# Performance work log

Measured on AMD Instinct MI355X. Metric: run time of the kernel, lower is better.

Reference implementation:

```python
import jax, jax.numpy as jnp
import numpy as np

B, S, H, R = 32, 1024, 768, 24
ATT_EPS = 1e10
LN_EPS = 1e-12


def setup_inputs() -> dict:
    key = jax.random.key(0)
    ks = jax.random.split(key, 20)
    sc = 0.02
    inp = {
        "relation": jax.random.randint(ks[0], (B, 1), 0, R),
        "last_hidden_size": jax.random.normal(ks[1], (B, S, H), dtype=jnp.float32),
        "sub_head": jax.random.randint(ks[2], (B, 1), 0, S),
        "sub_tail": jax.random.randint(ks[3], (B, 1), 0, S),
        "attention_mask": jnp.ones((B, S), dtype=jnp.float32),
        # learned parameters
        "rel_emb": jax.random.normal(ks[4], (R, H)) * sc,
        "W_rf": jax.random.normal(ks[5], (H, H)) * sc,
        "b_rf": jnp.zeros((H,), jnp.float32),
        "gamma": jnp.ones((H,), jnp.float32),
        "beta": jnp.zeros((H,), jnp.float32),
        "W_wd": jax.random.normal(ks[6], (H, 2 * H)) * sc,
        "W_bd": jax.random.normal(ks[7], (H, 2 * H)) * sc,
        "Wq": jax.random.normal(ks[8], (H, H)) * sc,
        "bq": jnp.zeros((H,), jnp.float32),
        "Wk": jax.random.normal(ks[9], (H, H)) * sc,
        "bk": jnp.zeros((H,), jnp.float32),
        "Wv": jax.random.normal(ks[10], (H, H)) * sc,
        "bv": jnp.zeros((H,), jnp.float32),
        "W_obj": jax.random.normal(ks[11], (1, H)) * sc,
        "b_obj": jnp.zeros((1,), jnp.float32),
    }
    return inp


def reference(relation, last_hidden_size, sub_head, sub_tail, attention_mask,
              rel_emb, W_rf, b_rf, gamma, beta, W_wd, W_bd,
              Wq, bq, Wk, bk, Wv, bv, W_obj, b_obj):
    # dropout layers are identity in eval mode
    # relation feature: embedding -> linear -> ReLU6   [B,1,H]
    rel_feature = jnp.clip(rel_emb[relation] @ W_rf.T + b_rf, 0.0, 6.0)
    # subject span features via gather                 [B,1,H]
    sh = jnp.take_along_axis(last_hidden_size, sub_head[:, :, None], axis=1)
    st = jnp.take_along_axis(last_hidden_size, sub_tail[:, :, None], axis=1)
    sub_feature = (sh + st) * 0.5
    cond = jnp.concatenate([rel_feature, sub_feature], axis=-1)  # [B,1,2H]

    # conditional layer norm: per-sample affine from condition
    weight = cond @ W_wd.T + gamma  # [B,1,H]
    bias = cond @ W_bd.T + beta     # [B,1,H]
    mean = jnp.mean(last_hidden_size, axis=-1, keepdims=True)
    ctr = last_hidden_size - mean
    var = jnp.mean(ctr * ctr, axis=-1, keepdims=True)
    x = ctr / jnp.sqrt(var + LN_EPS)
    x = x * weight + bias  # [B,S,H]

    # custom attention: ReLU-activated q/k/v, additive mask bias, residual
    q = jax.nn.relu(x @ Wq.T + bq)
    k = jax.nn.relu(x @ Wk.T + bk)
    v = jax.nn.relu(x @ Wv.T + bv)
    e = jnp.einsum('bsh,bth->bst', q, k)  # [B,S,S]
    e = e - ATT_EPS * (1.0 - attention_mask[:, None, :])
    a = jax.nn.softmax(e, axis=-1)
    hidden = jnp.einsum('bst,bth->bsh', a, v) + x  # residual

    pred_obj_head = jnp.squeeze(hidden @ W_obj.T + b_obj, axis=-1)  # [B,S]
    return pred_obj_head, hidden
```

## Files before the change

### kernel.cpp

```cpp
#include <hip/hip_runtime.h>

constexpr int NB  = 32;
constexpr int NS  = 1024;
constexpr int NH  = 768;
constexpr int NH2 = 1536;
constexpr int NQKV = 2304;
constexpr int NBS = NB * NS;

typedef __bf16 bf16x8 __attribute__((ext_vector_type(8)));
typedef float  f32x4  __attribute__((ext_vector_type(4)));
typedef unsigned short u16x8 __attribute__((ext_vector_type(8)));

__device__ __forceinline__ unsigned short f2bf(float f) {
  unsigned int u = __builtin_bit_cast(unsigned int, f);
  u += 0x7FFFu + ((u >> 16) & 1u);
  return (unsigned short)(u >> 16);
}
__device__ __forceinline__ float bf2f(unsigned short h) {
  return __builtin_bit_cast(float, ((unsigned int)h) << 16);
}

#define GLDS16(g, l)                                                         \
  __builtin_amdgcn_global_load_lds(                                          \
      (__attribute__((address_space(1))) void*)(g),                          \
      (__attribute__((address_space(3))) void*)(l), 16, 0, 0)

#define SBAR()    asm volatile("s_barrier" ::: "memory")
#define WAITVM6() asm volatile("s_waitcnt vmcnt(6)" ::: "memory")
#define WAITVM4() asm volatile("s_waitcnt vmcnt(4)" ::: "memory")
#define WAITVM0() asm volatile("s_waitcnt vmcnt(0)" ::: "memory")
#define LGKM0()                                                              \
  do {                                                                       \
    asm volatile("s_waitcnt lgkmcnt(0)" ::: "memory");                       \
    __builtin_amdgcn_sched_barrier(0);                                       \
  } while (0)

__launch_bounds__(256)
__global__ void cond_pre(const int* __restrict__ relation,
                         const float* __restrict__ h,
                         const int* __restrict__ subh,
                         const int* __restrict__ subt,
                         const float* __restrict__ rel_emb,
                         float* __restrict__ reT, float* __restrict__ condT) {
  const int b = blockIdx.x, t = threadIdx.x;
  const int r = relation[b], sh = subh[b], st = subt[b];
  for (int k = t; k < NH; k += 256) {
    reT[(size_t)k * NB + b] = rel_emb[(size_t)r * NH + k];
    condT[(size_t)(NH + k) * NB + b] =
        0.5f * (h[((size_t)b * NS + sh) * NH + k] +
                h[((size_t)b * NS + st) * NH + k]);
  }
}

__launch_bounds__(256)
__global__ void cond_rf(const float* __restrict__ W_rf,
                        const float* __restrict__ b_rf,
                        const float* __restrict__ reT,
                        float* __restrict__ condT) {
  const int t = threadIdx.x;
  const int b = t & 31, jl = t >> 5;
  const int j = blockIdx.x * 8 + jl;
  const float4* w4 = (const float4*)(W_rf + (size_t)j * NH);
  const float* rT = reT + b;
  float a0 = 0.f, a1 = 0.f;
  for (int k4 = 0; k4 < NH / 4; k4++) {
    float4 w = w4[k4];
    const float* c = rT + (size_t)(k4 * 4) * NB;
    a0 += w.x * c[0] + w.y * c[NB];
    a1 += w.z * c[2 * NB] + w.w * c[3 * NB];
  }
  float acc = a0 + a1 + b_rf[j];
  condT[(size_t)j * NB + b] = fminf(fmaxf(acc, 0.0f), 6.0f);
}

__launch_bounds__(256)
__global__ void cond_wb(const float* __restrict__ W_wd,
                        const float* __restrict__ W_bd,
                        const float* __restrict__ gamma,
                        const float* __restrict__ beta,
                        const float* __restrict__ condT,
                        float* __restrict__ wt, float* __restrict__ bs) {
  __shared__ float redW[128], redB[128];
  const int t = threadIdx.x;
  const int b = t & 31, jl = (t >> 5) & 3, ks = t >> 7;
  const int j = blockIdx.x * 4 + jl;
  const float4* ww = (const float4*)(W_wd + (size_t)j * NH2 + ks * NH);
  const float4* wb = (const float4*)(W_bd + (size_t)j * NH2 + ks * NH);
  const float* cT = condT + (size_t)ks * NH * NB + b;
  float aw0 = 0.f, aw1 = 0.f, ab0 = 0.f, ab1 = 0.f;
  for (int k4 = 0; k4 < NH / 4; k4++) {
    float4 w = ww[k4];
    float4 v = wb[k4];
    const float* c = cT + (size_t)(k4 * 4) * NB;
    float c0 = c[0], c1 = c[NB], c2 = c[2 * NB], c3 = c[3 * NB];
    aw0 += w.x * c0 + w.y * c1;
    aw1 += w.z * c2 + w.w * c3;
    ab0 += v.x * c0 + v.y * c1;
    ab1 += v.z * c2 + v.w * c3;
  }
  float aw = aw0 + aw1, ab = ab0 + ab1;
  if (ks == 1) {
    redW[t - 128] = aw;
    redB[t - 128] = ab;
  }
  __syncthreads();
  if (ks == 0) {
    aw += redW[t];
    ab += redB[t];
    wt[(size_t)b * NH + j] = aw + gamma[j];
    bs[(size_t)b * NH + j] = ab + beta[j];
  }
}

__launch_bounds__(64)
__global__ void ln_kernel(const float* __restrict__ h,
                          const float* __restrict__ wt,
                          const float* __restrict__ bs,
                          unsigned short* __restrict__ xbf) {
  const int row = blockIdx.x;
  const int b = row >> 10;
  const int lane = threadIdx.x;
  const float4* hr = (const float4*)(h + (size_t)row * NH);
  float4 v0 = hr[lane], v1 = hr[lane + 64], v2 = hr[lane + 128];
  float sum = 0.f, sq = 0.f;
  {
    sum += v0.x + v0.y + v0.z + v0.w;
    sq  += v0.x * v0.x + v0.y * v0.y + v0.z * v0.z + v0.w * v0.w;
    sum += v1.x + v1.y + v1.z + v1.w;
    sq  += v1.x * v1.x + v1.y * v1.y + v1.z * v1.z + v1.w * v1.w;
    sum += v2.x + v2.y + v2.z + v2.w;
    sq  += v2.x * v2.x + v2.y * v2.y + v2.z * v2.z + v2.w * v2.w;
  }
  for (int off = 32; off > 0; off >>= 1) {
    sum += __shfl_xor(sum, off, 64);
    sq  += __shfl_xor(sq, off, 64);
  }
  const float mean = sum * (1.0f / NH);
  const float var  = sq * (1.0f / NH) - mean * mean;
  const float rstd = rsqrtf(var + 1e-12f);
  const float4* wr = (const float4*)(wt + (size_t)b * NH);
  const float4* br = (const float4*)(bs + (size_t)b * NH);
  ushort4* xr = (ushort4*)(xbf + (size_t)row * NH);
#pragma unroll
  for (int i = 0; i < 3; i++) {
    float4 v = (i == 0) ? v0 : (i == 1) ? v1 : v2;
    float4 w = wr[lane + 64 * i];
    float4 bb = br[lane + 64 * i];
    ushort4 o;
    o.x = f2bf((v.x - mean) * rstd * w.x + bb.x);
    o.y = f2bf((v.y - mean) * rstd * w.y + bb.y);
    o.z = f2bf((v.z - mean) * rstd * w.z + bb.z);
    o.w = f2bf((v.w - mean) * rstd * w.w + bb.w);
    xr[lane + 64 * i] = o;
  }
}

__launch_bounds__(256)
__global__ void prep_w(const float* __restrict__ Wq, const float* __restrict__ bq,
                       const float* __restrict__ Wk, const float* __restrict__ bk,
                       const float* __restrict__ Wv, const float* __restrict__ bv,
                       unsigned short* __restrict__ Wcat, float* __restrict__ bcat) {
  const int row = blockIdx.x;
  const float* Wsrc;
  const float* bsrc;
  int r;
  if (row < NH) { Wsrc = Wq; bsrc = bq; r = row; }
  else if (row < NH2) { Wsrc = Wk; bsrc = bk; r = row - NH; }
  else { Wsrc = Wv; bsrc = bv; r = row - NH2; }
  for (int j = threadIdx.x; j < NH; j += 256)
    Wcat[(size_t)row * NH + j] = f2bf(Wsrc[(size_t)r * NH + j]);
  if (threadIdx.x == 0) bcat[row] = bsrc[r];
}

template <int TM, int OUTMODE, int RELU, int HASBIAS, int RES, int SPLIT3,
          int FPRED>
__launch_bounds__(512, 2)
__global__ void gemm256(const unsigned short* __restrict__ A, long long sAz, int lda,
                        const unsigned short* __restrict__ Bm, long long sBz, int ldb,
                        void* __restrict__ C, long long sCz, int ldc,
                        const float* __restrict__ bias,
                        const unsigned short* __restrict__ Res, long long sRz, int ldr,
                        int K, unsigned short* __restrict__ vTp,
                        const float* __restrict__ wobj,
                        const float* __restrict__ bobj,
                        float* __restrict__ pred) {
  extern __shared__ char lds[];
  const int t = threadIdx.x;
  const int z = blockIdx.z;
  int id = blockIdx.x + blockIdx.y * gridDim.x;
  {
    const int nwg = gridDim.x * gridDim.y;
    const int q = nwg >> 3, r = nwg & 7;
    const int xcd = id & 7, lid = id >> 3;
    id = (xcd < r ? xcd * (q + 1) : r * (q + 1) + (xcd - r) * q) + lid;
  }
  const int tileN = (id % gridDim.x) * 256;
  const int tileM = (id / gridDim.x) * TM;
  const unsigned short* Ab = A + (size_t)z * sAz + (size_t)tileM * lda;
  const unsigned short* Bb = Bm + (size_t)z * sBz + (size_t)tileN * ldb;

  const int lane = t & 63;
  const int w = t >> 6;
  const int wmr = w >> 2, wn = w & 3;
  const int lr = lane & 15, hi = lane >> 4;
  const int swz = (lr & 7) << 4;
  const int brow0 = (wn & 1) * 64;
  const int arow0 = (TM == 128) ? wmr * 64 : 0;
  constexpr int BBASE = (TM == 256) ? 65536 : 32768;

  const int sr = t >> 3;
  const int scc = (t & 7) ^ (sr & 7);

#define STAGEH(Gb, ld, kc, dst)                                             \
  do {                                                                      \
    GLDS16((Gb) + (size_t)sr * (ld) + (kc) + scc * 8, (dst) + (size_t)t * 16); \
    GLDS16((Gb) + (size_t)(64 + sr) * (ld) + (kc) + scc * 8,                \
           (dst) + 8192 + (size_t)t * 16);                                  \
  } while (0)

#define RD_BALL(Bh)                                                         \
  do {                                                                      \
    _Pragma("unroll") for (int nn_ = 0; nn_ < 4; nn_++)                     \
      _Pragma("unroll") for (int ks_ = 0; ks_ < 2; ks_++)                   \
        bF[nn_][ks_] = *(const bf16x8*)((Bh) + (brow0 + nn_ * 16 + lr) * 128 + \
                                        ((ks_ * 64 + hi * 16) ^ swz));      \
  } while (0)

#define RD_AH(m0, Ah)                                                       \
  do {                                                                      \
    _Pragma("unroll") for (int mm_ = 0; mm_ < 4; mm_++)                     \
      _Pragma("unroll") for (int ks_ = 0; ks_ < 2; ks_++)                   \
        aF[mm_][ks_] = *(const bf16x8*)((Ah) + ((arow0 + (m0) * 16 + mm_ * 16 + lr) * 128) + \
                                        ((ks_ * 64 + hi * 16) ^ swz));      \
  } while (0)

#define MFMAQ(mb, nb)                                                       \
  do {                                                                      \
    __builtin_amdgcn_s_setprio(1);                                          \
    _Pragma("unroll") for (int ks_ = 0; ks_ < 2; ks_++)                     \
      _Pragma("unroll") for (int mm_ = 0; mm_ < 4; mm_++)                   \
        _Pragma("unroll") for (int nn_ = 0; nn_ < 2; nn_++)                 \
          acc[(mb) + mm_][(nb) + nn_] = __builtin_amdgcn_mfma_f32_16x16x32_bf16( \
              aF[mm_][ks_], bF[(nb) + nn_][ks_], acc[(mb) + mm_][(nb) + nn_], \
              0, 0, 0);                                                     \
    __builtin_amdgcn_s_setprio(0);                                          \
  } while (0)

  f32x4 acc[TM / 32][4];
#pragma unroll
  for (int m = 0; m < TM / 32; m++)
#pragma unroll
    for (int n = 0; n < 4; n++) acc[m][n] = (f32x4)0.0f;

  const int NT = K >> 6;

  if (TM == 256) {
    STAGEH(Bb, ldb, 0, lds + BBASE);
    STAGEH(Bb + (size_t)128 * ldb, ldb, 0, lds + BBASE + 16384);
    STAGEH(Ab, lda, 0, lds);
    STAGEH(Ab + (size_t)128 * lda, lda, 0, lds + 16384);
    STAGEH(Bb, ldb, 64, lds + BBASE + 32768);
    STAGEH(Bb + (size_t)128 * ldb, ldb, 64, lds + BBASE + 32768 + 16384);
    STAGEH(Ab, lda, 64, lds + 32768);
    WAITVM6();
    SBAR();
    for (int kt = 0; kt < NT; kt++) {
      const int bc = kt & 1;
      const char* Ah = lds + bc * 32768 + wmr * 16384;
      const char* Bh = lds + BBASE + bc * 32768 + (wn >> 1) * 16384;
      bf16x8 aF[4][2], bF[4][2];
      RD_BALL(Bh);
      RD_AH(0, Ah);
      if (kt + 1 < NT)
        STAGEH(Ab + (size_t)128 * lda, lda, (kt + 1) * 64,
               lds + (bc ^ 1) * 32768 + 16384);
      SBAR();
      LGKM0();
      MFMAQ(0, 0);
      SBAR();
      if (kt + 2 < NT)
        STAGEH(Bb, ldb, (kt + 2) * 64, lds + BBASE + bc * 32768);
      SBAR();
      MFMAQ(0, 2);
      SBAR();
      RD_AH(4, Ah);
      if (kt + 2 < NT)
        STAGEH(Bb + (size_t)128 * ldb, ldb, (kt + 2) * 64,
               lds + BBASE + bc * 32768 + 16384);
      SBAR();
      LGKM0();
      MFMAQ(4, 2);
      SBAR();
      if (kt + 2 < NT)
        STAGEH(Ab, lda, (kt + 2) * 64, lds + bc * 32768);
      SBAR();
      MFMAQ(4, 0);
      if (kt + 2 < NT) {
        WAITVM6();
      } else if (kt + 1 < NT) {
        WAITVM0();
      }
      SBAR();
    }
  } else {
    STAGEH(Bb, ldb, 0, lds + BBASE);
    STAGEH(Bb + (size_t)128 * ldb, ldb, 0, lds + BBASE + 16384);
    STAGEH(Ab, lda, 0, lds);
    STAGEH(Bb, ldb, 64, lds + BBASE + 32768);
    STAGEH(Bb + (size_t)128 * ldb, ldb, 64, lds + BBASE + 32768 + 16384);
    WAITVM4();
    SBAR();
    for (int kt = 0; kt < NT; kt++) {
      const int bc = kt & 1;
      const char* Ah = lds + bc * 16384;
      const char* Bh = lds + BBASE + bc * 32768 + (wn >> 1) * 16384;
      bf16x8 aF[4][2], bF[4][2];
      RD_BALL(Bh);
      RD_AH(0, Ah);
      if (kt + 1 < NT)
        STAGEH(Ab, lda, (kt + 1) * 64, lds + (bc ^ 1) * 16384);
      SBAR();
      LGKM0();
      MFMAQ(0, 0);
      SBAR();
      if (kt + 2 < NT) {
        STAGEH(Bb, ldb, (kt + 2) * 64, lds + BBASE + bc * 32768);
        STAGEH(Bb + (size_t)128 * ldb, ldb, (kt + 2) * 64,
               lds + BBASE + bc * 32768 + 16384);
      }
      SBAR();
      MFMAQ(0, 2);
      if (kt + 2 < NT) {
        WAITVM4();
      } else if (kt + 1 < NT) {
        WAITVM0();
      }
      SBAR();
    }
  }

  const int row0 = tileM + wmr * ((TM == 256) ? 128 : 64);
  const int col0 = tileN + wn * 64;

  if (SPLIT3 && tileN >= NH2) {
    unsigned short* lt = (unsigned short*)lds;
    const int bz = tileM >> 10;
    const int sbase = tileM & (NS - 1);
    const int myhalf = wn >> 1;
#pragma unroll
    for (int half = 0; half < 2; half++) {
      if (myhalf == half) {
#pragma unroll
        for (int m = 0; m < TM / 32; m++) {
          const int lrow = (row0 - tileM) + m * 16 + hi * 4;
#pragma unroll
          for (int n = 0; n < 4; n++) {
            const int lcol = (wn & 1) * 64 + n * 16 + lr;
            const float bv = HASBIAS ? bias[col0 + n * 16 + lr] : 0.0f;
            f32x4 v = acc[m][n];
#pragma unroll
            for (int r = 0; r < 4; r++) {
              float x = v[r] + bv;
              if (RELU) x = fmaxf(x, 0.0f);
              lt[lcol * 264 + lrow + r] = f2bf(x);
            }
          }
        }
      }
      SBAR();
      {
        const int h = t >> 2;
        const int hglob = (tileN - NH2) + half * 128 + h;
        unsigned short* dst =
            vTp + ((size_t)bz * NH + hglob) * NS + sbase;
#pragma unroll
        for (int it = 0; it < 8; it++) {
          const int s = (t & 3) * 8 + it * 32;
          u16x8 vv = *(const u16x8*)&lt[h * 264 + s];
          *(u16x8*)(dst + s) = vv;
        }
      }
      SBAR();
    }
  } else {
#pragma unroll
    for (int m = 0; m < TM / 32; m++) {
      const int rowb = row0 + m * 16 + hi * 4;
      float psum[4] = {0.f, 0.f, 0.f, 0.f};
#pragma unroll
      for (int n = 0; n < 4; n++) {
        const int col = col0 + n * 16 + lr;
        const float bv = HASBIAS ? bias[col] : 0.0f;
        f32x4 v = acc[m][n];
#pragma unroll
        for (int r = 0; r < 4; r++) {
          float x = v[r] + bv;
          if (RELU) x = fmaxf(x, 0.0f);
          if (RES)
            x += bf2f(Res[(size_t)z * sRz + (size_t)(rowb + r) * ldr + col]);
          if (SPLIT3) {
            const int seg = col >= NH ? 1 : 0;
            ((unsigned short*)C)[(size_t)seg * NBS * NH +
                                 (size_t)(rowb + r) * NH + (col - seg * NH)] =
                f2bf(x);
          } else if (OUTMODE == 1) {
            ((unsigned short*)C)[(size_t)z * sCz + (size_t)(rowb + r) * ldc +
                                 col] = f2bf(x);
          } else if (OUTMODE == 2) {
            ((_Float16*)C)[(size_t)z * sCz + (size_t)(rowb + r) * ldc + col] =
                (_Float16)x;
          } else {
            ((float*)C)[(size_t)z * sCz + (size_t)(rowb + r) * ldc + col] = x;
          }
          if (FPRED) psum[r] += x * wobj[col];
        }
      }
      if (FPRED) {
#pragma unroll
        for (int r = 0; r < 4; r++) {
          float s = psum[r];
          s += __shfl_xor(s, 1, 64);
          s += __shfl_xor(s, 2, 64);
          s += __shfl_xor(s, 4, 64);
          s += __shfl_xor(s, 8, 64);
          if (lr == 0) {
            float add = s + ((tileN == 0 && wn == 0) ? bobj[0] : 0.0f);
            atomicAdd(pred + (size_t)z * NS + rowb + r, add);
          }
        }
      }
    }
  }
#undef STAGEH
#undef RD_BALL
#undef RD_AH
#undef MFMAQ
}

__launch_bounds__(256)
__global__ void softmax_kernel(const _Float16* __restrict__ e,
                               unsigned short* __restrict__ p,
                               const float* __restrict__ mask, int b0) {
  const int ri = blockIdx.x;
  const int lb = blockIdx.y;
  const int b = b0 + lb;
  const _Float16* row = e + ((size_t)lb * NS + ri) * NS;
  const int t = threadIdx.x;
  typedef _Float16 f16x4 __attribute__((ext_vector_type(4)));
  f16x4 u = ((const f16x4*)row)[t];
  float4 m = ((const float4*)(mask + (size_t)b * NS))[t];
  float v0 = (float)u[0] - 1e10f * (1.0f - m.x);
  float v1 = (float)u[1] - 1e10f * (1.0f - m.y);
  float v2 = (float)u[2] - 1e10f * (1.0f - m.z);
  float v3 = (float)u[3] - 1e10f * (1.0f - m.w);
  float mx = fmaxf(fmaxf(v0, v1), fmaxf(v2, v3));
  __shared__ float red[4];
  for (int off = 32; off > 0; off >>= 1) mx = fmaxf(mx, __shfl_xor(mx, off, 64));
  if ((t & 63) == 0) red[t >> 6] = mx;
  __syncthreads();
  mx = fmaxf(fmaxf(red[0], red[1]), fmaxf(red[2], red[3]));
  const float e0 = __expf(v0 - mx), e1 = __expf(v1 - mx);
  const float e2 = __expf(v2 - mx), e3 = __expf(v3 - mx);
  float sm = e0 + e1 + e2 + e3;
  __syncthreads();
  for (int off = 32; off > 0; off >>= 1) sm += __shfl_xor(sm, off, 64);
  if ((t & 63) == 0) red[t >> 6] = sm;
  __syncthreads();
  sm = red[0] + red[1] + red[2] + red[3];
  const float inv = 1.0f / sm;
  ushort4 o;
  o.x = f2bf(e0 * inv);
  o.y = f2bf(e1 * inv);
  o.z = f2bf(e2 * inv);
  o.w = f2bf(e3 * inv);
  ((ushort4*)(p + ((size_t)lb * NS + ri) * NS))[t] = o;
}

extern "C" void kernel_launch(void* const* d_in, const int* in_sizes, int n_in,
                              void* d_out, int out_size, void* d_ws,
                              size_t ws_size, hipStream_t stream) {
  const int* relation   = (const int*)d_in[0];
  const float* lhs      = (const float*)d_in[1];
  const int* sub_head   = (const int*)d_in[2];
  const int* sub_tail   = (const int*)d_in[3];
  const float* att_mask = (const float*)d_in[4];
  const float* rel_emb  = (const float*)d_in[5];
  const float* W_rf     = (const float*)d_in[6];
  const float* b_rf     = (const float*)d_in[7];
  const float* gamma    = (const float*)d_in[8];
  const float* beta     = (const float*)d_in[9];
  const float* W_wd     = (const float*)d_in[10];
  const float* W_bd     = (const float*)d_in[11];
  const float* Wq       = (const float*)d_in[12];
  const float* bq       = (const float*)d_in[13];
  const float* Wk       = (const float*)d_in[14];
  const float* bk       = (const float*)d_in[15];
  const float* Wv       = (const float*)d_in[16];
  const float* bv       = (const float*)d_in[17];
  const float* W_obj    = (const float*)d_in[18];
  const float* b_obj    = (const float*)d_in[19];

  char* ws = (char*)d_ws;
  unsigned short* Wcat = (unsigned short*)(ws + 0);
  float* bcat  = (float*)(ws + 3538944);
  float* wt    = (float*)(ws + 3548160);
  float* bs    = (float*)(ws + 3646464);
  float* reT   = (float*)(ws + 3744768);
  float* condT = (float*)(ws + 3843072);
  unsigned short* xbf = (unsigned short*)(ws + 4039680);
  unsigned short* qkv = (unsigned short*)(ws + 54371328);
  unsigned short* vT  = (unsigned short*)(ws + 155034624);
  char* attbuf = ws + 205366272;

  float* out_pred = (float*)d_out;
  float* out_hidden = out_pred + NBS;

  const size_t fixed = 205366272ull;
  size_t avail = ws_size > fixed ? ws_size - fixed : 0;
  int CB = 32;
  while (CB > 1 && (size_t)CB * ((size_t)NS * NS * 2 + (size_t)NS * NS * 2) > avail)
    CB >>= 1;
  _Float16* ebuf = (_Float16*)attbuf;
  unsigned short* pbuf =
      (unsigned short*)(attbuf + (size_t)CB * NS * NS * 2);

  prep_w<<<dim3(NQKV), dim3(256), 0, stream>>>(Wq, bq, Wk, bk, Wv, bv, Wcat, bcat);
  cond_pre<<<dim3(NB), dim3(256), 0, stream>>>(relation, lhs, sub_head, sub_tail,
                                               rel_emb, reT, condT);
  cond_rf<<<dim3(NH / 8), dim3(256), 0, stream>>>(W_rf, b_rf, reT, condT);
  cond_wb<<<dim3(NH / 4), dim3(256), 0, stream>>>(W_wd, W_bd, gamma, beta, condT,
                                                  wt, bs);
  ln_kernel<<<dim3(NBS), dim3(64), 0, stream>>>(lhs, wt, bs, xbf);
  hipMemsetAsync(out_pred, 0, (size_t)NBS * sizeof(float), stream);

  gemm256<256, 1, 1, 1, 0, 1, 0>
      <<<dim3(NQKV / 256, NBS / 256, 1), dim3(512), 131072, stream>>>(
          xbf, 0, NH, Wcat, 0, NH, qkv, 0, NH, bcat, nullptr, 0, 0, NH, vT,
          nullptr, nullptr, nullptr);

  for (int b0 = 0; b0 < NB; b0 += CB) {
    gemm256<256, 2, 0, 0, 0, 0, 0>
        <<<dim3(NS / 256, NS / 256, CB), dim3(512), 131072, stream>>>(
            qkv + (size_t)b0 * NS * NH, (long long)NS * NH, NH,
            qkv + (size_t)NBS * NH + (size_t)b0 * NS * NH, (long long)NS * NH, NH,
            ebuf, (long long)NS * NS, NS, nullptr, nullptr, 0, 0, NH, nullptr,
            nullptr, nullptr, nullptr);
    softmax_kernel<<<dim3(NS, CB), dim3(256), 0, stream>>>(ebuf, pbuf, att_mask,
                                                           b0);
    gemm256<128, 0, 0, 0, 1, 0, 1>
        <<<dim3(NH / 256, NS / 128, CB), dim3(512), 98304, stream>>>(
            pbuf, (long long)NS * NS, NS,
            vT + (size_t)b0 * NH * NS, (long long)NH * NS, NS,
            out_hidden + (size_t)b0 * NS * NH, (long long)NS * NH, NH, nullptr,
            xbf + (size_t)b0 * NS * NH, (long long)NS * NH, NH, NS, nullptr,
            W_obj, b_obj, out_pred + (size_t)b0 * NS);
  }
}
```

Baseline: 454.1 us.

## Fuse softmax exponentiation into PV GEMM and mask into QK epilogue

Replaces the full softmax kernel, which wrote a normalized bf16 probability matrix, with a row-statistics kernel that writes only the per-row max and inverse sum. The PV GEMM now reads the raw fp16 scores, applies exp(x - max) while loading A fragments, and multiplies by the inverse sum in its epilogue. The attention-mask bias moves into the QK GEMM epilogue. This removes one full write of the probability matrix to memory, but the exponentials are recomputed redundantly by every wave and N-tile that shares a row, right in the MFMA inner loop.

```diff
diff --git a/kernel.cpp b/kernel.cpp
--- a/kernel.cpp
+++ b/kernel.cpp
@@ -10,6 +10,8 @@
 typedef __bf16 bf16x8 __attribute__((ext_vector_type(8)));
 typedef float  f32x4  __attribute__((ext_vector_type(4)));
 typedef unsigned short u16x8 __attribute__((ext_vector_type(8)));
+typedef _Float16 f16x8 __attribute__((ext_vector_type(8)));
+typedef _Float16 f16x4 __attribute__((ext_vector_type(4)));
 
 __device__ __forceinline__ unsigned short f2bf(float f) {
   unsigned int u = __builtin_bit_cast(unsigned int, f);
@@ -173,7 +175,7 @@
 }
 
 template <int TM, int OUTMODE, int RELU, int HASBIAS, int RES, int SPLIT3,
-          int FPRED>
+          int FPRED, int MASKB, int PVEXP>
 __launch_bounds__(512, 2)
 __global__ void gemm256(const unsigned short* __restrict__ A, long long sAz, int lda,
                         const unsigned short* __restrict__ Bm, long long sBz, int ldb,
@@ -181,6 +183,9 @@
                         const float* __restrict__ bias,
                         const unsigned short* __restrict__ Res, long long sRz, int ldr,
                         int K, unsigned short* __restrict__ vTp,
+                        const float* __restrict__ maskp,
+                        const float* __restrict__ rmax,
+                        const float* __restrict__ rinv,
                         const float* __restrict__ wobj,
                         const float* __restrict__ bobj,
                         float* __restrict__ pred) {
@@ -211,6 +216,13 @@
   const int sr = t >> 3;
   const int scc = (t & 7) ^ (sr & 7);
 
+  float mxv[4];
+  if (PVEXP) {
+#pragma unroll
+    for (int m = 0; m < 4; m++)
+      mxv[m] = rmax[(size_t)z * NS + tileM + arow0 + m * 16 + lr];
+  }
+
 #define STAGEH(Gb, ld, kc, dst)                                             \
   do {                                                                      \
     GLDS16((Gb) + (size_t)sr * (ld) + (kc) + scc * 8, (dst) + (size_t)t * 16); \
@@ -229,9 +241,19 @@
 #define RD_AH(m0, Ah)                                                       \
   do {                                                                      \
     _Pragma("unroll") for (int mm_ = 0; mm_ < 4; mm_++)                     \
-      _Pragma("unroll") for (int ks_ = 0; ks_ < 2; ks_++)                   \
-        aF[mm_][ks_] = *(const bf16x8*)((Ah) + ((arow0 + (m0) * 16 + mm_ * 16 + lr) * 128) + \
-                                        ((ks_ * 64 + hi * 16) ^ swz));      \
+      _Pragma("unroll") for (int ks_ = 0; ks_ < 2; ks_++) {                 \
+        const char* ap_ = (Ah) + ((arow0 + (m0) * 16 + mm_ * 16 + lr) * 128) + \
+                          ((ks_ * 64 + hi * 16) ^ swz);                     \
+        if (PVEXP) {                                                        \
+          f16x8 raw_ = *(const f16x8*)ap_;                                  \
+          u16x8 pb_;                                                        \
+          _Pragma("unroll") for (int j_ = 0; j_ < 8; j_++)                  \
+            pb_[j_] = f2bf(__expf((float)raw_[j_] - mxv[mm_]));             \
+          aF[mm_][ks_] = __builtin_bit_cast(bf16x8, pb_);                   \
+        } else {                                                            \
+          aF[mm_][ks_] = *(const bf16x8*)ap_;                               \
+        }                                                                   \
+      }                                                                     \
   } while (0)
 
 #define MFMAQ(mb, nb)                                                       \
@@ -387,6 +409,9 @@
     for (int m = 0; m < TM / 32; m++) {
       const int rowb = row0 + m * 16 + hi * 4;
       float psum[4] = {0.f, 0.f, 0.f, 0.f};
+      float4 isv;
+      if (PVEXP)
+        isv = *(const float4*)(rinv + (size_t)z * NS + rowb);
 #pragma unroll
       for (int n = 0; n < 4; n++) {
         const int col = col0 + n * 16 + lr;
@@ -395,7 +420,9 @@
 #pragma unroll
         for (int r = 0; r < 4; r++) {
           float x = v[r] + bv;
+          if (PVEXP) x *= ((const float*)&isv)[r];
           if (RELU) x = fmaxf(x, 0.0f);
+          if (MASKB) x -= 1e10f * (1.0f - maskp[(size_t)z * NS + col]);
           if (RES)
             x += bf2f(Res[(size_t)z * sRz + (size_t)(rowb + r) * ldr + col]);
           if (SPLIT3) {
@@ -438,42 +465,32 @@
 }
 
 __launch_bounds__(256)
-__global__ void softmax_kernel(const _Float16* __restrict__ e,
-                               unsigned short* __restrict__ p,
-                               const float* __restrict__ mask, int b0) {
+__global__ void rowstats_kernel(const _Float16* __restrict__ e,
+                                float* __restrict__ rmax,
+                                float* __restrict__ rinv) {
   const int ri = blockIdx.x;
   const int lb = blockIdx.y;
-  const int b = b0 + lb;
   const _Float16* row = e + ((size_t)lb * NS + ri) * NS;
   const int t = threadIdx.x;
-  typedef _Float16 f16x4 __attribute__((ext_vector_type(4)));
   f16x4 u = ((const f16x4*)row)[t];
-  float4 m = ((const float4*)(mask + (size_t)b * NS))[t];
-  float v0 = (float)u[0] - 1e10f * (1.0f - m.x);
-  float v1 = (float)u[1] - 1e10f * (1.0f - m.y);
-  float v2 = (float)u[2] - 1e10f * (1.0f - m.z);
-  float v3 = (float)u[3] - 1e10f * (1.0f - m.w);
+  float v0 = (float)u[0], v1 = (float)u[1], v2 = (float)u[2], v3 = (float)u[3];
   float mx = fmaxf(fmaxf(v0, v1), fmaxf(v2, v3));
   __shared__ float red[4];
   for (int off = 32; off > 0; off >>= 1) mx = fmaxf(mx, __shfl_xor(mx, off, 64));
   if ((t & 63) == 0) red[t >> 6] = mx;
   __syncthreads();
   mx = fmaxf(fmaxf(red[0], red[1]), fmaxf(red[2], red[3]));
-  const float e0 = __expf(v0 - mx), e1 = __expf(v1 - mx);
-  const float e2 = __expf(v2 - mx), e3 = __expf(v3 - mx);
-  float sm = e0 + e1 + e2 + e3;
+  float sm = __expf(v0 - mx) + __expf(v1 - mx) + __expf(v2 - mx) +
+             __expf(v3 - mx);
   __syncthreads();
   for (int off = 32; off > 0; off >>= 1) sm += __shfl_xor(sm, off, 64);
   if ((t & 63) == 0) red[t >> 6] = sm;
   __syncthreads();
-  sm = red[0] + red[1] + red[2] + red[3];
-  const float inv = 1.0f / sm;
-  ushort4 o;
-  o.x = f2bf(e0 * inv);
-  o.y = f2bf(e1 * inv);
-  o.z = f2bf(e2 * inv);
-  o.w = f2bf(e3 * inv);
-  ((ushort4*)(p + ((size_t)lb * NS + ri) * NS))[t] = o;
+  if (t == 0) {
+    sm = red[0] + red[1] + red[2] + red[3];
+    rmax[(size_t)lb * NS + ri] = mx;
+    rinv[(size_t)lb * NS + ri] = 1.0f / sm;
+  }
 }
 
 extern "C" void kernel_launch(void* const* d_in, const int* in_sizes, int n_in,
@@ -518,11 +535,12 @@
   const size_t fixed = 205366272ull;
   size_t avail = ws_size > fixed ? ws_size - fixed : 0;
   int CB = 32;
-  while (CB > 1 && (size_t)CB * ((size_t)NS * NS * 2 + (size_t)NS * NS * 2) > avail)
+  while (CB > 1 &&
+         (size_t)CB * ((size_t)NS * NS * 2 + (size_t)NS * 8) > avail)
     CB >>= 1;
   _Float16* ebuf = (_Float16*)attbuf;
-  unsigned short* pbuf =
-      (unsigned short*)(attbuf + (size_t)CB * NS * NS * 2);
+  float* rmax = (float*)(attbuf + (size_t)CB * NS * NS * 2);
+  float* rinv = rmax + (size_t)CB * NS;
 
   prep_w<<<dim3(NQKV), dim3(256), 0, stream>>>(Wq, bq, Wk, bk, Wv, bv, Wcat, bcat);
   cond_pre<<<dim3(NB), dim3(256), 0, stream>>>(relation, lhs, sub_head, sub_tail,
@@ -533,26 +551,26 @@
   ln_kernel<<<dim3(NBS), dim3(64), 0, stream>>>(lhs, wt, bs, xbf);
   hipMemsetAsync(out_pred, 0, (size_t)NBS * sizeof(float), stream);
 
-  gemm256<256, 1, 1, 1, 0, 1, 0>
+  gemm256<256, 1, 1, 1, 0, 1, 0, 0, 0>
       <<<dim3(NQKV / 256, NBS / 256, 1), dim3(512), 131072, stream>>>(
           xbf, 0, NH, Wcat, 0, NH, qkv, 0, NH, bcat, nullptr, 0, 0, NH, vT,
-          nullptr, nullptr, nullptr);
+          nullptr, nullptr, nullptr, nullptr, nullptr, nullptr);
 
   for (int b0 = 0; b0 < NB; b0 += CB) {
-    gemm256<256, 2, 0, 0, 0, 0, 0>
+    gemm256<256, 2, 0, 0, 0, 0, 0, 1, 0>
         <<<dim3(NS / 256, NS / 256, CB), dim3(512), 131072, stream>>>(
             qkv + (size_t)b0 * NS * NH, (long long)NS * NH, NH,
             qkv + (size_t)NBS * NH + (size_t)b0 * NS * NH, (long long)NS * NH, NH,
             ebuf, (long long)NS * NS, NS, nullptr, nullptr, 0, 0, NH, nullptr,
-            nullptr, nullptr, nullptr);
-    softmax_kernel<<<dim3(NS, CB), dim3(256), 0, stream>>>(ebuf, pbuf, att_mask,
-                                                           b0);
-    gemm256<128, 0, 0, 0, 1, 0, 1>
+            att_mask + (size_t)b0 * NS, nullptr, nullptr, nullptr, nullptr,
+            nullptr);
+    rowstats_kernel<<<dim3(NS, CB), dim3(256), 0, stream>>>(ebuf, rmax, rinv);
+    gemm256<128, 0, 0, 0, 1, 0, 1, 0, 1>
         <<<dim3(NH / 256, NS / 128, CB), dim3(512), 98304, stream>>>(
-            pbuf, (long long)NS * NS, NS,
+            (const unsigned short*)ebuf, (long long)NS * NS, NS,
             vT + (size_t)b0 * NH * NS, (long long)NH * NS, NS,
             out_hidden + (size_t)b0 * NS * NH, (long long)NS * NH, NH, nullptr,
             xbf + (size_t)b0 * NS * NH, (long long)NS * NH, NH, NS, nullptr,
-            W_obj, b_obj, out_pred + (size_t)b0 * NS);
-  }
-}
+            nullptr, rmax, rinv, W_obj, b_obj, out_pred + (size_t)b0 * NS);
+  }
+}
```

After: 492.5 us. +8.5%, slower.
